# Kernel optimization log

Hardware: AMD Instinct MI355X
Metric: run time of the kernel (lower is better)

## Reference

```python
import jax, jax.numpy as jnp
import numpy as np

GROUPS = 16
EPS = 1e-6


def group_norm(x, gamma, beta):
    b, c, h, w = x.shape
    xg = x.reshape(b, GROUPS, c // GROUPS, h, w)
    mean = xg.mean(axis=(2, 3, 4), keepdims=True)
    var = xg.var(axis=(2, 3, 4), keepdims=True)
    xn = ((xg - mean) * jax.lax.rsqrt(var + EPS)).reshape(b, c, h, w)
    return xn * gamma[None, :, None, None] + beta[None, :, None, None]


def conv1x1(x, w, b):
    # x: [B,C,H,W], w: [O,C], b: [O]
    return jnp.einsum('bchw,oc->bohw', x, w) + b[None, :, None, None]


def setup_inputs() -> dict:
    key = jax.random.key(0)
    ks = jax.random.split(key, 10)
    C = 256
    x = jax.random.normal(ks[0], (4, C, 64, 64), dtype=jnp.float32)
    s = 1.0 / np.sqrt(C)
    return {
        'x': x,
        'gamma': jnp.ones((C,), jnp.float32),
        'beta': jnp.zeros((C,), jnp.float32),
        'wq': jax.random.normal(ks[1], (C, C), jnp.float32) * s,
        'bq': jnp.zeros((C,), jnp.float32),
        'wk': jax.random.normal(ks[2], (C, C), jnp.float32) * s,
        'bk': jnp.zeros((C,), jnp.float32),
        'wv': jax.random.normal(ks[3], (C, C), jnp.float32) * s,
        'bv': jnp.zeros((C,), jnp.float32),
        'wp': jax.random.normal(ks[4], (C, C), jnp.float32) * s,
        'bp': jnp.zeros((C,), jnp.float32),
    }


def reference(x, gamma, beta, wq, bq, wk, bk, wv, bv, wp, bp):
    b, c, h, w = x.shape
    hn = group_norm(x, gamma, beta)
    q = conv1x1(hn, wq, bq).reshape(b, c, h * w)   # [B,C,N]
    k = conv1x1(hn, wk, bk).reshape(b, c, h * w)
    v = conv1x1(hn, wv, bv).reshape(b, c, h * w)
    # scores[b,i,j] = sum_c q[b,c,i] * k[b,c,j], scaled by c^-0.5
    scores = jnp.einsum('bci,bcj->bij', q, k) * (c ** -0.5)
    attn = jax.nn.softmax(scores, axis=2)           # [B,N,N]
    # h_out[b,c,i] = sum_j v[b,c,j] * attn[b,i,j]
    h_out = jnp.einsum('bcj,bij->bci', v, attn).reshape(b, c, h, w)
    return x + conv1x1(h_out, wp, bp)
```

## Files before the change

kernel.cpp:

```cpp
#include <hip/hip_runtime.h>

#define B_ 4
#define C_ 256
#define N_ 4096
#define K2_ 0.09016844f
#define THR_ 64.0f

typedef __attribute__((ext_vector_type(8))) short short8;
typedef __attribute__((ext_vector_type(4))) float f32x4;
typedef __attribute__((ext_vector_type(16))) float f32x16;
typedef __attribute__((ext_vector_type(4))) unsigned int uint4v;

static __device__ __forceinline__ short f2bf(float f) {
  union { float f; unsigned u; } v; v.f = f;
  unsigned r = v.u + 0x7FFFu + ((v.u >> 16) & 1u);
  return (short)(r >> 16);
}
static __device__ __forceinline__ float bf2f(short s) {
  union { unsigned u; float f; } v; v.u = ((unsigned)(unsigned short)s) << 16;
  return v.f;
}
static __device__ __forceinline__ f32x4 mfma16(short8 a, short8 b, f32x4 c) {
  return __builtin_amdgcn_mfma_f32_16x16x32_bf16(a, b, c, 0, 0, 0);
}
static __device__ __forceinline__ f32x16 mfma32(short8 a, short8 b, f32x16 c) {
  return __builtin_amdgcn_mfma_f32_32x32x16_bf16(a, b, c, 0, 0, 0);
}
static __device__ __forceinline__ unsigned cvtpk(float lo, float hi) {
  unsigned r;
  asm("v_cvt_pk_bf16_f32 %0, %1, %2" : "=v"(r) : "v"(lo), "v"(hi));
  return r;
}
static __device__ __forceinline__ void plswap(unsigned& a, unsigned& b) {
  asm volatile("v_permlane32_swap_b32 %0, %1" : "+v"(a), "+v"(b));
}
static __device__ __forceinline__ void gload16(const void* g, void* l) {
  __builtin_amdgcn_global_load_lds(
      (const __attribute__((address_space(1))) unsigned int*)g,
      (__attribute__((address_space(3))) unsigned int*)l, 16, 0, 0);
}

__global__ __launch_bounds__(256) void gn_stats1(const float* __restrict__ x,
                                                 float2* __restrict__ part) {
  int bg = blockIdx.x >> 2, ch = blockIdx.x & 3;
  const float* xp = x + (long)bg * 65536 + ch * 16384;
  int t = threadIdx.x, lane = t & 63, w = t >> 6;
  float s = 0.f, ss = 0.f;
  for (int e = t * 4; e < 16384; e += 1024) {
    f32x4 v = *(const f32x4*)(xp + e);
    s += (v[0] + v[1]) + (v[2] + v[3]);
    ss += (v[0] * v[0] + v[1] * v[1]) + (v[2] * v[2] + v[3] * v[3]);
  }
  for (int off = 1; off < 64; off <<= 1) {
    s += __shfl_xor(s, off);
    ss += __shfl_xor(ss, off);
  }
  __shared__ float rs[4], rq[4];
  if (lane == 0) { rs[w] = s; rq[w] = ss; }
  __syncthreads();
  if (t == 0)
    part[blockIdx.x] = make_float2((rs[0] + rs[1]) + (rs[2] + rs[3]),
                                   (rq[0] + rq[1]) + (rq[2] + rq[3]));
}

__global__ __launch_bounds__(256) void gn_norm(const float* __restrict__ x,
                                               const float* __restrict__ gamma,
                                               const float* __restrict__ beta,
                                               const float2* __restrict__ part,
                                               short* __restrict__ hn) {
  int ic = blockIdx.x, g = blockIdx.y, b = blockIdx.z;
  int bg = b * 16 + g;
  float2 q0 = part[bg * 4], q1 = part[bg * 4 + 1], q2 = part[bg * 4 + 2], q3 = part[bg * 4 + 3];
  float s = (q0.x + q1.x) + (q2.x + q3.x);
  float ss = (q0.y + q1.y) + (q2.y + q3.y);
  float mean = s * (1.f / 65536.f);
  float rstd = rsqrtf(ss * (1.f / 65536.f) - mean * mean + 1e-6f);
  int t = threadIdx.x;
  int i = ic * 256 + t;
  __shared__ short Ls[16][256];
#pragma unroll
  for (int cl = 0; cl < 16; cl++) {
    int c = g * 16 + cl;
    float v = x[((long)(b * 256 + c)) * N_ + i];
    Ls[cl][t] = f2bf((v - mean) * rstd * gamma[c] + beta[c]);
  }
  __syncthreads();
  short8 v0, v1;
#pragma unroll
  for (int q = 0; q < 8; q++) { v0[q] = Ls[q][t]; v1[q] = Ls[8 + q][t]; }
  short* dst = hn + ((long)b * N_ + ic * 256 + t) * C_ + g * 16;
  *(short8*)dst = v0;
  *(short8*)(dst + 8) = v1;
}

__global__ __launch_bounds__(256) void cast_w(const float* __restrict__ wq,
                                              const float* __restrict__ wk,
                                              const float* __restrict__ wv,
                                              const float* __restrict__ wp,
                                              short* __restrict__ out) {
  int idx = blockIdx.x * 256 + threadIdx.x;
  int which = idx >> 16, e = idx & 65535;
  const float* src = which == 0 ? wq : which == 1 ? wk : which == 2 ? wv : wp;
  out[(which << 16) + e] = f2bf(src[e]);
}

__global__ __launch_bounds__(256) void gemm_qkv(const short* __restrict__ hn,
                                                const short* __restrict__ wqkv,
                                                const float* __restrict__ bq,
                                                const float* __restrict__ bk,
                                                const float* __restrict__ bv,
                                                short* __restrict__ qT,
                                                short* __restrict__ kT,
                                                short* __restrict__ vbM) {
  __shared__ __align__(16) short As[2][128 * 32];
  __shared__ __align__(16) short Bs[2][128 * 32];
  const int bz = blockIdx.z;
  const int n0 = blockIdx.x * 128;
  const int m0 = blockIdx.y * 128;
  const int t = threadIdx.x, lane = t & 63, w = t >> 6;
  const int wm = (w >> 1) * 64, wn = (w & 1) * 64;
  const short* Ab = hn + (long)bz * N_ * C_;
  f32x4 acc[4][4];
#pragma unroll
  for (int m = 0; m < 4; m++)
#pragma unroll
    for (int n = 0; n < 4; n++) acc[m][n] = (f32x4)0.f;
  const int g16 = (lane >> 4) * 16;

  auto stage = [&](int kt8, int buf) {
    int kt = kt8 * 32;
#pragma unroll
    for (int s = 0; s < 2; s++) {
      int q = w * 2 + s;
      int flat = q * 1024 + lane * 16;
      int row = flat >> 6, c = flat & 63;
      int cs = c ^ ((row & 3) << 4);
      gload16((const char*)Ab + ((long)(m0 + row) * 256 + kt) * 2 + cs, (char*)As[buf] + flat);
      gload16((const char*)wqkv + ((long)(n0 + row) * 256 + kt) * 2 + cs, (char*)Bs[buf] + flat);
    }
  };

  stage(0, 0);
  __syncthreads();
  for (int kt8 = 0; kt8 < 8; kt8++) {
    int cur = kt8 & 1;
    if (kt8 < 7) stage(kt8 + 1, cur ^ 1);
    short8 af[4], bf[4];
#pragma unroll
    for (int m = 0; m < 4; m++) {
      int row = wm + m * 16 + (lane & 15);
      af[m] = *(const short8*)(&As[cur][0] + row * 32 + ((g16 ^ ((row & 3) << 4)) >> 1));
    }
#pragma unroll
    for (int n = 0; n < 4; n++) {
      int row = wn + n * 16 + (lane & 15);
      bf[n] = *(const short8*)(&Bs[cur][0] + row * 32 + ((g16 ^ ((row & 3) << 4)) >> 1));
    }
    __builtin_amdgcn_s_setprio(1);
#pragma unroll
    for (int m = 0; m < 4; m++)
#pragma unroll
      for (int n = 0; n < 4; n++) acc[m][n] = mfma16(af[m], bf[n], acc[m][n]);
    __builtin_amdgcn_s_setprio(0);
    __syncthreads();
  }

  int seg = n0 >> 8;
  const float* bias = seg == 0 ? bq : seg == 1 ? bk : bv;
#pragma unroll
  for (int m = 0; m < 4; m++)
#pragma unroll
    for (int n = 0; n < 4; n++)
#pragma unroll
      for (int r = 0; r < 4; r++) {
        int row = m0 + wm + m * 16 + ((lane >> 4) << 2) + r;
        int colg = n0 + wn + n * 16 + (lane & 15);
        int coll = colg & 255;
        float vv = acc[m][n][r] + bias[coll];
        if (seg == 2) vbM[(long)bz * N_ * C_ + (long)coll * N_ + row] = f2bf(vv);
        else (seg == 0 ? qT : kT)[(long)bz * N_ * C_ + (long)row * 256 + coll] = f2bf(vv);
      }
}

__global__ __launch_bounds__(256) void gemm_proj(const short* __restrict__ wp,
                                                 const short* __restrict__ hT,
                                                 const float* __restrict__ bp,
                                                 const float* __restrict__ x,
                                                 float* __restrict__ out) {
  __shared__ __align__(16) short As[2][128 * 32];
  __shared__ __align__(16) short Bs[2][128 * 32];
  const int bz = blockIdx.z;
  const int n0 = blockIdx.x * 128;
  const int m0 = blockIdx.y * 128;
  const int t = threadIdx.x, lane = t & 63, w = t >> 6;
  const int wm = (w >> 1) * 64, wn = (w & 1) * 64;
  const short* Bb = hT + (long)bz * N_ * C_;
  f32x4 acc[4][4];
#pragma unroll
  for (int m = 0; m < 4; m++)
#pragma unroll
    for (int n = 0; n < 4; n++) acc[m][n] = (f32x4)0.f;
  const int g16 = (lane >> 4) * 16;

  auto stage = [&](int kt8, int buf) {
    int kt = kt8 * 32;
#pragma unroll
    for (int s = 0; s < 2; s++) {
      int q = w * 2 + s;
      int flat = q * 1024 + lane * 16;
      int row = flat >> 6, c = flat & 63;
      int cs = c ^ ((row & 3) << 4);
      gload16((const char*)wp + ((long)(m0 + row) * 256 + kt) * 2 + cs, (char*)As[buf] + flat);
      gload16((const char*)Bb + ((long)(n0 + row) * 256 + kt) * 2 + cs, (char*)Bs[buf] + flat);
    }
  };

  stage(0, 0);
  __syncthreads();
  for (int kt8 = 0; kt8 < 8; kt8++) {
    int cur = kt8 & 1;
    if (kt8 < 7) stage(kt8 + 1, cur ^ 1);
    short8 af[4], bf[4];
#pragma unroll
    for (int m = 0; m < 4; m++) {
      int row = wm + m * 16 + (lane & 15);
      af[m] = *(const short8*)(&As[cur][0] + row * 32 + ((g16 ^ ((row & 3) << 4)) >> 1));
    }
#pragma unroll
    for (int n = 0; n < 4; n++) {
      int row = wn + n * 16 + (lane & 15);
      bf[n] = *(const short8*)(&Bs[cur][0] + row * 32 + ((g16 ^ ((row & 3) << 4)) >> 1));
    }
    __builtin_amdgcn_s_setprio(1);
#pragma unroll
    for (int m = 0; m < 4; m++)
#pragma unroll
      for (int n = 0; n < 4; n++) acc[m][n] = mfma16(af[m], bf[n], acc[m][n]);
    __builtin_amdgcn_s_setprio(0);
    __syncthreads();
  }

#pragma unroll
  for (int m = 0; m < 4; m++)
#pragma unroll
    for (int n = 0; n < 4; n++)
#pragma unroll
      for (int r = 0; r < 4; r++) {
        int row = m0 + wm + m * 16 + ((lane >> 4) << 2) + r;
        int col = n0 + wn + n * 16 + (lane & 15);
        long idx = (long)bz * N_ * C_ + (long)row * N_ + col;
        out[idx] = acc[m][n][r] + bp[row] + x[idx];
      }
}

__global__ __launch_bounds__(256, 2) void attn_kernel(
    const short* __restrict__ qT, const short* __restrict__ kT,
    const short* __restrict__ vM, short* __restrict__ P0, short* __restrict__ P1,
    short* __restrict__ P2, short* __restrict__ P3, float2* __restrict__ ml, int S) {
  __shared__ __align__(16) char kv[3 * 16384];
  __shared__ float cbr[4][32];

  const int nwg = 128 * S;
  const int id = blockIdx.x;
  const int nid = (id & 7) * (nwg >> 3) + (id >> 3);
  const int itile = nid & 31;
  const int bjs = nid >> 5;
  const int js = bjs % S;
  const int b = bjs / S;

  const int t = threadIdx.x, lane = t & 63, w = t >> 6;
  const int hi = lane >> 5, li = lane & 31;
  const int hi16 = hi * 16;
  const int lsw = li << 4;
  const long bNC = (long)b * N_ * C_;
  const short* qb = qT + bNC;
  const char* kb = (const char*)(kT + bNC);
  const char* vbp = (const char*)(vM + bNC);
  const int i0 = itile * 128 + w * 32;
  const int jbase = js * (N_ / S);
  const int NIT = (N_ / S) / 32;

  short8 qf[16];
  {
    const short* qp = qb + (long)(i0 + li) * C_ + hi * 8;
#pragma unroll
    for (int s = 0; s < 16; s++) qf[s] = *(const short8*)(qp + s * 16);
  }

  f32x16 acco[8];
#pragma unroll
  for (int cb = 0; cb < 8; cb++) acco[cb] = (f32x16)0.f;
  float m_run = -3e38f, l_run = 0.f;

  auto stage = [&](int it, int vb) {
    const int j0 = jbase + it * 32;
    char* Kd = kv;
    char* Vd = kv + 16384 + vb * 16384;
#pragma unroll
    for (int p = 0; p < 4; p++) {
      int flat = p * 4096 + t * 16;
      int rk = flat >> 9;
      int cO = (flat & 511) ^ ((rk & 31) << 4);
      gload16(kb + (long)(j0 + rk) * 512 + cO, Kd + flat);
    }
#pragma unroll
    for (int p = 0; p < 4; p++) {
      int flat = p * 4096 + t * 16;
      int rv = flat >> 9;
      int cO = (flat & 511) ^ ((rv & 31) << 4);
      int c = rv + ((cO >> 6) << 5);
      int off = cO & 63;
      gload16(vbp + (long)c * 8192 + (long)j0 * 2 + off, Vd + flat);
    }
  };

  auto smpack = [&](f32x16& accs, short8& paA, short8& paB) {
    float pmax = fmaxf(fmaxf(accs[0], accs[1]), accs[2]);
#pragma unroll
    for (int r = 3; r < 16; r += 2) pmax = fmaxf(fmaxf(accs[r], accs[r + 1 < 16 ? r + 1 : r]), pmax);
    pmax = fmaxf(pmax, __shfl_xor(pmax, 32));
    if (__any(pmax > m_run + THR_)) {
      float mnew = fmaxf(m_run, pmax);
      float corr = exp2f((m_run - mnew) * K2_);
      m_run = mnew;
      l_run *= corr;
      if (lane < 32) cbr[w][li] = corr;
      asm volatile("s_waitcnt lgkmcnt(0)" ::: "memory");
      f32x4 c4[4];
#pragma unroll
      for (int g = 0; g < 4; g++) c4[g] = *(const f32x4*)&cbr[w][g * 8 + hi * 4];
#pragma unroll
      for (int cb = 0; cb < 8; cb++)
#pragma unroll
        for (int r = 0; r < 16; r++) acco[cb][r] *= c4[r >> 2][r & 3];
    }
    const float mk = m_run * K2_;
    float p[16];
#pragma unroll
    for (int r = 0; r < 16; r++) {
      p[r] = exp2f(fmaf(accs[r], K2_, -mk));
      l_run += p[r];
    }
    unsigned a0 = cvtpk(p[0], p[1]), b0 = cvtpk(p[4], p[5]);
    unsigned a1 = cvtpk(p[2], p[3]), b1 = cvtpk(p[6], p[7]);
    plswap(a0, b0); plswap(a1, b1);
    uint4v u0 = {a0, a1, b0, b1};
    paA = __builtin_bit_cast(short8, u0);
    unsigned a2 = cvtpk(p[8], p[9]), b2 = cvtpk(p[12], p[13]);
    unsigned a3 = cvtpk(p[10], p[11]), b3 = cvtpk(p[14], p[15]);
    plswap(a2, b2); plswap(a3, b3);
    uint4v u1 = {a2, a3, b2, b3};
    paB = __builtin_bit_cast(short8, u1);
  };

  const char* Kr = kv + li * 512;

  stage(0, 0);
  __syncthreads();
  f32x16 accs = (f32x16)0.f;
  __builtin_amdgcn_s_setprio(1);
#pragma unroll
  for (int s = 0; s < 16; s++) {
    short8 kf = *(const short8*)(Kr + ((s * 32 + hi16) ^ lsw));
    accs = mfma32(kf, qf[s], accs);
  }
  __builtin_amdgcn_s_setprio(0);

  short8 pa0, pa1;
  for (int it = 1; it < NIT; it++) {
    __syncthreads();
    stage(it, it & 1);
    smpack(accs, pa0, pa1);
    __syncthreads();
    const char* Vr = kv + 16384 + ((it - 1) & 1) * 16384 + li * 512;
    f32x16 a2 = (f32x16)0.f;
    __builtin_amdgcn_s_setprio(1);
#pragma unroll
    for (int u = 0; u < 8; u++) {
      short8 kfa = *(const short8*)(Kr + (((2 * u) * 32 + hi16) ^ lsw));
      a2 = mfma32(kfa, qf[2 * u], a2);
      short8 vf0 = *(const short8*)(Vr + ((u * 64 + hi16) ^ lsw));
      acco[u] = mfma32(pa0, vf0, acco[u]);
      short8 kfb = *(const short8*)(Kr + (((2 * u + 1) * 32 + hi16) ^ lsw));
      a2 = mfma32(kfb, qf[2 * u + 1], a2);
      short8 vf1 = *(const short8*)(Vr + ((u * 64 + 32 + hi16) ^ lsw));
      acco[u] = mfma32(pa1, vf1, acco[u]);
    }
    __builtin_amdgcn_s_setprio(0);
    accs = a2;
  }

  smpack(accs, pa0, pa1);
  {
    const char* Vr = kv + 16384 + ((NIT - 1) & 1) * 16384 + li * 512;
    __builtin_amdgcn_s_setprio(1);
#pragma unroll
    for (int cb = 0; cb < 8; cb++) {
      short8 vf0 = *(const short8*)(Vr + ((cb * 64 + hi16) ^ lsw));
      acco[cb] = mfma32(pa0, vf0, acco[cb]);
      short8 vf1 = *(const short8*)(Vr + ((cb * 64 + 32 + hi16) ^ lsw));
      acco[cb] = mfma32(pa1, vf1, acco[cb]);
    }
    __builtin_amdgcn_s_setprio(0);
  }

  l_run += __shfl_xor(l_run, 32);
  float inv = 1.f / l_run;
  if (lane < 32) cbr[w][li] = inv;
  asm volatile("s_waitcnt lgkmcnt(0)" ::: "memory");
  f32x4 i4[4];
#pragma unroll
  for (int g = 0; g < 4; g++) i4[g] = *(const f32x4*)&cbr[w][g * 8 + hi * 4];

  short* Op = (js == 0) ? P0 : (js == 1) ? P1 : (js == 2) ? P2 : P3;
  short* ob = Op + bNC;
#pragma unroll
  for (int cb = 0; cb < 8; cb++)
#pragma unroll
    for (int r = 0; r < 16; r++) {
      int i = i0 + (r & 3) + 8 * (r >> 2) + 4 * hi;
      ob[(long)i * C_ + cb * 32 + li] = f2bf(acco[cb][r] * i4[r >> 2][r & 3]);
    }
  if (lane < 32)
    ml[(long)js * (B_ * N_) + b * N_ + i0 + li] = make_float2(m_run * K2_, l_run);
}

__global__ __launch_bounds__(256) void combine(const short* __restrict__ p0,
                                               const short* __restrict__ p1,
                                               const short* __restrict__ p2,
                                               const short* __restrict__ p3,
                                               const float2* __restrict__ ml, int S,
                                               short* __restrict__ hT) {
  int idx = blockIdx.x * 256 + threadIdx.x;
  int row = idx >> 5, c0 = (idx & 31) * 8;
  float2 m0 = ml[row], m1 = ml[16384 + row];
  float mmax = fmaxf(m0.x, m1.x);
  float2 m2 = m0, m3 = m0;
  if (S == 4) {
    m2 = ml[2 * 16384 + row];
    m3 = ml[3 * 16384 + row];
    mmax = fmaxf(mmax, fmaxf(m2.x, m3.x));
  }
  float w0 = m0.y * exp2f(m0.x - mmax);
  float w1 = m1.y * exp2f(m1.x - mmax);
  float w2 = 0.f, w3 = 0.f;
  if (S == 4) { w2 = m2.y * exp2f(m2.x - mmax); w3 = m3.y * exp2f(m3.x - mmax); }
  float inv = 1.f / ((w0 + w1) + (w2 + w3));
  w0 *= inv; w1 *= inv; w2 *= inv; w3 *= inv;
  long off = (long)row * 256 + c0;
  short8 u0 = *(const short8*)(p0 + off);
  short8 u1 = *(const short8*)(p1 + off);
  short8 o;
  if (S == 4) {
    short8 u2 = *(const short8*)(p2 + off);
    short8 u3 = *(const short8*)(p3 + off);
#pragma unroll
    for (int j = 0; j < 8; j++)
      o[j] = f2bf((w0 * bf2f(u0[j]) + w1 * bf2f(u1[j])) +
                  (w2 * bf2f(u2[j]) + w3 * bf2f(u3[j])));
  } else {
#pragma unroll
    for (int j = 0; j < 8; j++) o[j] = f2bf(w0 * bf2f(u0[j]) + w1 * bf2f(u1[j]));
  }
  *(short8*)(hT + off) = o;
}

extern "C" void kernel_launch(void* const* d_in, const int* in_sizes, int n_in,
                              void* d_out, int out_size, void* d_ws, size_t ws_size,
                              hipStream_t stream) {
  const float* x = (const float*)d_in[0];
  const float* gamma = (const float*)d_in[1];
  const float* beta = (const float*)d_in[2];
  const float* wq = (const float*)d_in[3];
  const float* bq = (const float*)d_in[4];
  const float* wk = (const float*)d_in[5];
  const float* bk = (const float*)d_in[6];
  const float* wv = (const float*)d_in[7];
  const float* bv = (const float*)d_in[8];
  const float* wp = (const float*)d_in[9];
  const float* bp = (const float*)d_in[10];

  char* ws = (char*)d_ws;
  short* hn = (short*)ws;
  short* qT = (short*)(ws + (size_t)8388608);
  short* kT = (short*)(ws + (size_t)16777216);
  short* vb = (short*)(ws + (size_t)25165824);
  short* wqkv = (short*)(ws + (size_t)33554432);
  short* wpb = wqkv + 3 * 65536;
  float2* part = (float2*)(ws + (size_t)34078720);
  float2* ml = (float2*)(ws + (size_t)34080768);
  short* P1 = (short*)d_out;
  short* P2 = (short*)d_out + 4194304;
  short* P3 = (short*)(ws + (size_t)34605056);
  const int S = (ws_size >= (size_t)43000000) ? 4 : 2;
  if (S == 2) { P2 = hn; P3 = hn; }

  gn_stats1<<<256, 256, 0, stream>>>(x, part);
  gn_norm<<<dim3(16, 16, 4), 256, 0, stream>>>(x, gamma, beta, part, hn);
  cast_w<<<1024, 256, 0, stream>>>(wq, wk, wv, wp, wqkv);

  gemm_qkv<<<dim3(6, 32, 4), 256, 0, stream>>>(hn, wqkv, bq, bk, bv, qT, kT, vb);

  attn_kernel<<<dim3(128 * S), 256, 0, stream>>>(qT, kT, vb, hn , P1, P2, P3, ml, S);
  combine<<<2048, 256, 0, stream>>>(hn, P1, P2, P3, ml, S, hn );

  gemm_proj<<<dim3(32, 2, 4), 256, 0, stream>>>(wpb, hn, bp, x, (float*)d_out);
}
```

Baseline: 173.4 us.

## Triple-buffer GEMM loads with partial vmcnt waits and split attention barriers

```diff
diff --git a/kernel.cpp b/kernel.cpp
--- a/kernel.cpp
+++ b/kernel.cpp
@@ -112,8 +112,8 @@
                                                 short* __restrict__ qT,
                                                 short* __restrict__ kT,
                                                 short* __restrict__ vbM) {
-  __shared__ __align__(16) short As[2][128 * 32];
-  __shared__ __align__(16) short Bs[2][128 * 32];
+  __shared__ __align__(16) short As[3][128 * 32];
+  __shared__ __align__(16) short Bs[3][128 * 32];
   const int bz = blockIdx.z;
   const int n0 = blockIdx.x * 128;
   const int m0 = blockIdx.y * 128;
@@ -141,10 +141,16 @@
   };
 
   stage(0, 0);
-  __syncthreads();
   for (int kt8 = 0; kt8 < 8; kt8++) {
-    int cur = kt8 & 1;
-    if (kt8 < 7) stage(kt8 + 1, cur ^ 1);
+    const int cur = kt8 % 3;
+    if (kt8 < 7) {
+      stage(kt8 + 1, (kt8 + 1) % 3);
+      asm volatile("s_waitcnt vmcnt(4)" ::: "memory");
+    } else {
+      asm volatile("s_waitcnt vmcnt(0)" ::: "memory");
+    }
+    __builtin_amdgcn_s_barrier();
+    __builtin_amdgcn_sched_barrier(0);
     short8 af[4], bf[4];
 #pragma unroll
     for (int m = 0; m < 4; m++) {
@@ -162,7 +168,6 @@
 #pragma unroll
       for (int n = 0; n < 4; n++) acc[m][n] = mfma16(af[m], bf[n], acc[m][n]);
     __builtin_amdgcn_s_setprio(0);
-    __syncthreads();
   }
 
   int seg = n0 >> 8;
@@ -187,8 +192,8 @@
                                                  const float* __restrict__ bp,
                                                  const float* __restrict__ x,
                                                  float* __restrict__ out) {
-  __shared__ __align__(16) short As[2][128 * 32];
-  __shared__ __align__(16) short Bs[2][128 * 32];
+  __shared__ __align__(16) short As[3][128 * 32];
+  __shared__ __align__(16) short Bs[3][128 * 32];
   const int bz = blockIdx.z;
   const int n0 = blockIdx.x * 128;
   const int m0 = blockIdx.y * 128;
@@ -216,10 +221,16 @@
   };
 
   stage(0, 0);
-  __syncthreads();
   for (int kt8 = 0; kt8 < 8; kt8++) {
-    int cur = kt8 & 1;
-    if (kt8 < 7) stage(kt8 + 1, cur ^ 1);
+    const int cur = kt8 % 3;
+    if (kt8 < 7) {
+      stage(kt8 + 1, (kt8 + 1) % 3);
+      asm volatile("s_waitcnt vmcnt(4)" ::: "memory");
+    } else {
+      asm volatile("s_waitcnt vmcnt(0)" ::: "memory");
+    }
+    __builtin_amdgcn_s_barrier();
+    __builtin_amdgcn_sched_barrier(0);
     short8 af[4], bf[4];
 #pragma unroll
     for (int m = 0; m < 4; m++) {
@@ -237,7 +248,6 @@
 #pragma unroll
       for (int n = 0; n < 4; n++) acc[m][n] = mfma16(af[m], bf[n], acc[m][n]);
     __builtin_amdgcn_s_setprio(0);
-    __syncthreads();
   }
 
 #pragma unroll
@@ -315,9 +325,12 @@
   };
 
   auto smpack = [&](f32x16& accs, short8& paA, short8& paB) {
-    float pmax = fmaxf(fmaxf(accs[0], accs[1]), accs[2]);
-#pragma unroll
-    for (int r = 3; r < 16; r += 2) pmax = fmaxf(fmaxf(accs[r], accs[r + 1 < 16 ? r + 1 : r]), pmax);
+    float pm[8];
+#pragma unroll
+    for (int r = 0; r < 8; r++) pm[r] = fmaxf(accs[2 * r], accs[2 * r + 1]);
+#pragma unroll
+    for (int r = 0; r < 4; r++) pm[r] = fmaxf(pm[2 * r], pm[2 * r + 1]);
+    float pmax = fmaxf(fmaxf(pm[0], pm[1]), fmaxf(pm[2], pm[3]));
     pmax = fmaxf(pmax, __shfl_xor(pmax, 32));
     if (__any(pmax > m_run + THR_)) {
       float mnew = fmaxf(m_run, pmax);
@@ -356,22 +369,34 @@
   const char* Kr = kv + li * 512;
 
   stage(0, 0);
-  __syncthreads();
-  f32x16 accs = (f32x16)0.f;
-  __builtin_amdgcn_s_setprio(1);
-#pragma unroll
-  for (int s = 0; s < 16; s++) {
-    short8 kf = *(const short8*)(Kr + ((s * 32 + hi16) ^ lsw));
-    accs = mfma32(kf, qf[s], accs);
-  }
-  __builtin_amdgcn_s_setprio(0);
+  asm volatile("s_waitcnt vmcnt(0)" ::: "memory");
+  __builtin_amdgcn_s_barrier();
+  __builtin_amdgcn_sched_barrier(0);
+  f32x16 accs;
+  {
+    f32x16 ae = (f32x16)0.f, ao = (f32x16)0.f;
+    __builtin_amdgcn_s_setprio(1);
+#pragma unroll
+    for (int u = 0; u < 8; u++) {
+      short8 k0 = *(const short8*)(Kr + (((2 * u) * 32 + hi16) ^ lsw));
+      ae = mfma32(k0, qf[2 * u], ae);
+      short8 k1 = *(const short8*)(Kr + (((2 * u + 1) * 32 + hi16) ^ lsw));
+      ao = mfma32(k1, qf[2 * u + 1], ao);
+    }
+    __builtin_amdgcn_s_setprio(0);
+    accs = ae + ao;
+  }
 
   short8 pa0, pa1;
   for (int it = 1; it < NIT; it++) {
-    __syncthreads();
+    asm volatile("s_waitcnt lgkmcnt(0)" ::: "memory");
+    __builtin_amdgcn_s_barrier();
+    __builtin_amdgcn_sched_barrier(0);
     stage(it, it & 1);
     smpack(accs, pa0, pa1);
-    __syncthreads();
+    asm volatile("s_waitcnt vmcnt(4)" ::: "memory");
+    __builtin_amdgcn_s_barrier();
+    __builtin_amdgcn_sched_barrier(0);
     const char* Vr = kv + 16384 + ((it - 1) & 1) * 16384 + li * 512;
     f32x16 a2 = (f32x16)0.f;
     __builtin_amdgcn_s_setprio(1);
@@ -391,6 +416,9 @@
   }
 
   smpack(accs, pa0, pa1);
+  asm volatile("s_waitcnt vmcnt(0)" ::: "memory");
+  __builtin_amdgcn_s_barrier();
+  __builtin_amdgcn_sched_barrier(0);
   {
     const char* Vr = kv + 16384 + ((NIT - 1) & 1) * 16384 + li * 512;
     __builtin_amdgcn_s_setprio(1);
```

New measurement: 172.7 us. Within noise of the previous version (-0.4%).
